# Kernel optimization log

Measured on AMD Instinct MI355X. Metric: run time of the kernel, lower is better.

## Reference

```python
import jax, jax.numpy as jnp
import numpy as np
import math

B, S, E = 4, 1024, 1024
H = 16
HD = E // H            # 64
HD2 = HD // 2          # 32
DEPTH = 12 - 1
LAMBDA_INIT = 0.8 - 0.6 * math.exp(-0.3 * DEPTH)
EPS = 1e-5


def setup_inputs() -> dict:
    key = jax.random.key(0)
    ks = jax.random.split(key, 16)
    std = 1.0 / math.sqrt(E)
    inp = {
        "hidden_states": jax.random.normal(ks[0], (B, S, E), jnp.float32),
        "q_w": jax.random.normal(ks[1], (E, E), jnp.float32) * std,
        "q_b": jnp.zeros((E,), jnp.float32),
        "k_w": jax.random.normal(ks[2], (E, E), jnp.float32) * std,
        "k_b": jnp.zeros((E,), jnp.float32),
        "v_w": jax.random.normal(ks[3], (E, E), jnp.float32) * std,
        "v_b": jnp.zeros((E,), jnp.float32),
        "o_w": jax.random.normal(ks[4], (E, E), jnp.float32) * std,
        "o_b": jnp.zeros((E,), jnp.float32),
        "lambda_q1": jax.random.normal(ks[5], (HD2,), jnp.float32) * 0.1,
        "lambda_k1": jax.random.normal(ks[6], (HD2,), jnp.float32) * 0.1,
        "lambda_q2": jax.random.normal(ks[7], (HD2,), jnp.float32) * 0.1,
        "lambda_k2": jax.random.normal(ks[8], (HD2,), jnp.float32) * 0.1,
        "subln_w": jnp.ones((HD,), jnp.float32),
    }
    return inp


def reference(hidden_states, q_w, q_b, k_w, k_b, v_w, v_b, o_w, o_b,
              lambda_q1, lambda_k1, lambda_q2, lambda_k2, subln_w):
    b, s, _ = hidden_states.shape
    # projections (torch Linear: x @ W.T + b)
    q = hidden_states @ q_w.T + q_b
    k = hidden_states @ k_w.T + k_b
    v = hidden_states @ v_w.T + v_b
    # split q/k into 2*H heads of dim HD2; v into H heads of dim HD
    q = q.reshape(b, s, 2 * H, HD2).transpose(0, 2, 1, 3)   # [B,2H,S,HD2]
    k = k.reshape(b, s, 2 * H, HD2).transpose(0, 2, 1, 3)   # [B,2H,S,HD2]
    v = v.reshape(b, s, H, HD).transpose(0, 2, 1, 3)        # [B,H,S,HD]
    # scores scaled by sqrt(head_dim) (full head_dim, per source)
    scores = jnp.einsum('bhqd,bhkd->bhqk', q, k) / math.sqrt(HD)
    scores = jnp.nan_to_num(scores)
    attn_w = jax.nn.softmax(scores.astype(jnp.float32), axis=-1).astype(scores.dtype)
    lam1 = jnp.exp(jnp.sum(lambda_q1 * lambda_k1))
    lam2 = jnp.exp(jnp.sum(lambda_q2 * lambda_k2))
    lam = lam1 - lam2 + LAMBDA_INIT
    attn_w = attn_w.reshape(b, H, 2, s, s)
    diff_w = attn_w[:, :, 0] - lam * attn_w[:, :, 1]        # [B,H,S,S]
    attn = jnp.einsum('bhqk,bhkd->bhqd', diff_w, v)          # [B,H,S,HD]
    # RMSNorm over head dim, elementwise affine
    attn = attn * jax.lax.rsqrt(jnp.mean(attn * attn, axis=-1, keepdims=True) + EPS) * subln_w
    attn = attn * (1.0 - LAMBDA_INIT)
    attn = attn.transpose(0, 2, 1, 3).reshape(b, s, H * HD)
    out = attn @ o_w.T + o_b
    return out, diff_w
```

## Files before the change

### kernel.cpp

```cpp
#include <hip/hip_runtime.h>

typedef __attribute__((ext_vector_type(8))) short short8;
typedef __attribute__((ext_vector_type(4))) float floatx4;

#define MFMA16(a, b, c) __builtin_amdgcn_mfma_f32_16x16x32_bf16((a), (b), (c), 0, 0, 0)

#define LAMBDA_INIT_F 0.777870099559256f
#define ONE_MINUS_LAMBDA_F 0.222129900440744f

static __device__ __forceinline__ unsigned short f2bf(float f) {
  union { float f; unsigned int u; } v; v.f = f;
  unsigned int r = v.u + 0x7FFFu + ((v.u >> 16) & 1u);
  return (unsigned short)(r >> 16);
}

__global__ __launch_bounds__(256) void cvt_f32_bf16(const float* __restrict__ in,
                                                    unsigned short* __restrict__ out,
                                                    int n) {
  int i = blockIdx.x * 256 + threadIdx.x;
  if (i < n) out[i] = f2bf(in[i]);
}

template <int MODE>
__global__ __launch_bounds__(256) void gemm_bt(const unsigned short* __restrict__ A,
                                               const unsigned short* __restrict__ Bt,
                                               const float* __restrict__ bias,
                                               void* __restrict__ out,
                                               int M, int N, int K) {
  __shared__ unsigned short As[64][40];
  __shared__ unsigned short Bs[64][40];
  const int tid = threadIdx.x;
  const int m0 = blockIdx.y * 64;
  const int n0 = blockIdx.x * 64;
  const int w = tid >> 6, lane = tid & 63;
  const int wm = (w >> 1) * 32, wn = (w & 1) * 32;
  const int lrow = lane & 15, quad = lane >> 4;

  floatx4 acc[2][2];
  for (int i = 0; i < 2; i++)
    for (int j = 0; j < 2; j++)
      acc[i][j] = (floatx4){0.f, 0.f, 0.f, 0.f};

  const int ldr = tid >> 2;
  const int ldc = (tid & 3) * 8;

  for (int k0 = 0; k0 < K; k0 += 32) {
    short8 av = *(const short8*)(A + (size_t)(m0 + ldr) * K + k0 + ldc);
    short8 bv = *(const short8*)(Bt + (size_t)(n0 + ldr) * K + k0 + ldc);
    *(short8*)(&As[ldr][ldc]) = av;
    *(short8*)(&Bs[ldr][ldc]) = bv;
    __syncthreads();
    short8 a0 = *(const short8*)(&As[wm + lrow][quad * 8]);
    short8 a1 = *(const short8*)(&As[wm + 16 + lrow][quad * 8]);
    short8 b0 = *(const short8*)(&Bs[wn + lrow][quad * 8]);
    short8 b1 = *(const short8*)(&Bs[wn + 16 + lrow][quad * 8]);
    acc[0][0] = MFMA16(a0, b0, acc[0][0]);
    acc[0][1] = MFMA16(a0, b1, acc[0][1]);
    acc[1][0] = MFMA16(a1, b0, acc[1][0]);
    acc[1][1] = MFMA16(a1, b1, acc[1][1]);
    __syncthreads();
  }

  for (int mi = 0; mi < 2; mi++)
    for (int ni = 0; ni < 2; ni++)
      for (int r = 0; r < 4; r++) {
        int row = m0 + wm + mi * 16 + quad * 4 + r;
        int col = n0 + wn + ni * 16 + lrow;
        float v = acc[mi][ni][r] + bias[col];
        if (MODE == 1) {
          int b = row >> 10, s = row & 1023, h2 = col >> 5, d = col & 31;
          ((unsigned short*)out)[((((size_t)(b * 32 + h2)) << 10) + s) * 32 + d] = f2bf(v);
        } else if (MODE == 2) {
          int b = row >> 10, s = row & 1023, h = col >> 6, d = col & 63;
          ((unsigned short*)out)[((((size_t)(b * 16 + h)) * 64 + d) << 10) + s] = f2bf(v);
        } else {
          ((float*)out)[(size_t)row * N + col] = v;
        }
      }
}

__global__ __launch_bounds__(256) void attn_stats(const unsigned short* __restrict__ qh,
                                                  const unsigned short* __restrict__ kh,
                                                  float* __restrict__ stat_m,
                                                  float* __restrict__ stat_l) {
  const int W = blockIdx.x * 4 + (threadIdx.x >> 6);
  const int lane = threadIdx.x & 63;
  const int chunk = W & 63;
  const int bh = W >> 6;
  const int b = bh >> 4, h = bh & 15;
  const int lrow = lane & 15, quad = lane >> 4;
  const int r0 = chunk * 16;

  const unsigned short* q1 = qh + ((((size_t)(b * 32 + 2 * h)) << 10) + r0) * 32;
  const unsigned short* q2 = qh + ((((size_t)(b * 32 + 2 * h + 1)) << 10) + r0) * 32;
  const unsigned short* k1 = kh + (((size_t)(b * 32 + 2 * h)) << 10) * 32;
  const unsigned short* k2 = kh + (((size_t)(b * 32 + 2 * h + 1)) << 10) * 32;

  short8 a1 = *(const short8*)(q1 + lrow * 32 + quad * 8);
  short8 a2 = *(const short8*)(q2 + lrow * 32 + quad * 8);

  float m1[4], l1[4], m2[4], l2[4];
  for (int r = 0; r < 4; r++) { m1[r] = -1e30f; l1[r] = 0.f; m2[r] = -1e30f; l2[r] = 0.f; }

  for (int c = 0; c < 64; c++) {
    short8 bk1 = *(const short8*)(k1 + (c * 16 + lrow) * 32 + quad * 8);
    short8 bk2 = *(const short8*)(k2 + (c * 16 + lrow) * 32 + quad * 8);
    floatx4 z = (floatx4){0.f, 0.f, 0.f, 0.f};
    floatx4 s1 = MFMA16(a1, bk1, z);
    floatx4 s2 = MFMA16(a2, bk2, z);
    for (int r = 0; r < 4; r++) {
      float v1 = s1[r] * 0.125f;
      float nm1 = fmaxf(m1[r], v1);
      l1[r] = l1[r] * __expf(m1[r] - nm1) + __expf(v1 - nm1);
      m1[r] = nm1;
      float v2 = s2[r] * 0.125f;
      float nm2 = fmaxf(m2[r], v2);
      l2[r] = l2[r] * __expf(m2[r] - nm2) + __expf(v2 - nm2);
      m2[r] = nm2;
    }
  }
  for (int off = 1; off < 16; off <<= 1) {
    for (int r = 0; r < 4; r++) {
      float om = __shfl_xor(m1[r], off);
      float ol = __shfl_xor(l1[r], off);
      float nm = fmaxf(m1[r], om);
      l1[r] = l1[r] * __expf(m1[r] - nm) + ol * __expf(om - nm);
      m1[r] = nm;
      om = __shfl_xor(m2[r], off);
      ol = __shfl_xor(l2[r], off);
      nm = fmaxf(m2[r], om);
      l2[r] = l2[r] * __expf(m2[r] - nm) + ol * __expf(om - nm);
      m2[r] = nm;
    }
  }
  if (lrow == 0) {
    for (int r = 0; r < 4; r++) {
      int row = r0 + quad * 4 + r;
      size_t i1 = (((size_t)(b * 32 + 2 * h)) << 10) + row;
      size_t i2 = (((size_t)(b * 32 + 2 * h + 1)) << 10) + row;
      stat_m[i1] = m1[r]; stat_l[i1] = l1[r];
      stat_m[i2] = m2[r]; stat_l[i2] = l2[r];
    }
  }
}

__global__ __launch_bounds__(256) void attn_pass2(const unsigned short* __restrict__ qh,
                                                  const unsigned short* __restrict__ kh,
                                                  const unsigned short* __restrict__ vt,
                                                  const float* __restrict__ stat_m,
                                                  const float* __restrict__ stat_l,
                                                  const float* __restrict__ lq1,
                                                  const float* __restrict__ lk1,
                                                  const float* __restrict__ lq2,
                                                  const float* __restrict__ lk2,
                                                  const float* __restrict__ subln,
                                                  float* __restrict__ diffw,
                                                  unsigned short* __restrict__ attn_out) {
  __shared__ unsigned short ds[4][16][40];
  const int wid = threadIdx.x >> 6;
  const int W = blockIdx.x * 4 + wid;
  const int lane = threadIdx.x & 63;
  const int chunk = W & 63;
  const int bh = W >> 6;
  const int b = bh >> 4, h = bh & 15;
  const int lrow = lane & 15, quad = lane >> 4;
  const int r0 = chunk * 16;

  float sl1 = 0.f, sl2 = 0.f;
  for (int i = 0; i < 32; i++) { sl1 += lq1[i] * lk1[i]; sl2 += lq2[i] * lk2[i]; }
  const float lam = __expf(sl1) - __expf(sl2) + LAMBDA_INIT_F;

  const unsigned short* q1 = qh + ((((size_t)(b * 32 + 2 * h)) << 10) + r0) * 32;
  const unsigned short* q2 = qh + ((((size_t)(b * 32 + 2 * h + 1)) << 10) + r0) * 32;
  const unsigned short* k1 = kh + (((size_t)(b * 32 + 2 * h)) << 10) * 32;
  const unsigned short* k2 = kh + (((size_t)(b * 32 + 2 * h + 1)) << 10) * 32;
  const unsigned short* vth = vt + (((size_t)(b * 16 + h)) << 16);

  short8 a1 = *(const short8*)(q1 + lrow * 32 + quad * 8);
  short8 a2 = *(const short8*)(q2 + lrow * 32 + quad * 8);

  float em1[4], il1[4], em2[4], il2[4];
  for (int r = 0; r < 4; r++) {
    int row = r0 + quad * 4 + r;
    size_t i1 = (((size_t)(b * 32 + 2 * h)) << 10) + row;
    size_t i2 = (((size_t)(b * 32 + 2 * h + 1)) << 10) + row;
    em1[r] = stat_m[i1]; il1[r] = 1.f / stat_l[i1];
    em2[r] = stat_m[i2]; il2[r] = 1.f / stat_l[i2];
  }

  floatx4 accO[4];
  for (int nt = 0; nt < 4; nt++) accO[nt] = (floatx4){0.f, 0.f, 0.f, 0.f};

  float* dwbase = diffw + (((size_t)bh) << 20) + (size_t)r0 * 1024;

  for (int c2 = 0; c2 < 32; c2++) {
    for (int cc = 0; cc < 2; cc++) {
      int c = c2 * 2 + cc;
      short8 bk1 = *(const short8*)(k1 + (c * 16 + lrow) * 32 + quad * 8);
      short8 bk2 = *(const short8*)(k2 + (c * 16 + lrow) * 32 + quad * 8);
      floatx4 z = (floatx4){0.f, 0.f, 0.f, 0.f};
      floatx4 s1 = MFMA16(a1, bk1, z);
      floatx4 s2 = MFMA16(a2, bk2, z);
      for (int r = 0; r < 4; r++) {
        float p1 = __expf(s1[r] * 0.125f - em1[r]) * il1[r];
        float p2 = __expf(s2[r] * 0.125f - em2[r]) * il2[r];
        float d = p1 - lam * p2;
        dwbase[(size_t)(quad * 4 + r) * 1024 + c * 16 + lrow] = d;
        ds[wid][quad * 4 + r][cc * 16 + lrow] = f2bf(d);
      }
    }
    short8 ad = *(const short8*)(&ds[wid][lrow][quad * 8]);
    for (int nt = 0; nt < 4; nt++) {
      short8 bv = *(const short8*)(vth + (((size_t)(nt * 16 + lrow)) << 10) + c2 * 32 + quad * 8);
      accO[nt] = MFMA16(ad, bv, accO[nt]);
    }
  }

  float rs[4];
  for (int r = 0; r < 4; r++) {
    float s = 0.f;
    for (int nt = 0; nt < 4; nt++) s += accO[nt][r] * accO[nt][r];
    for (int off = 1; off < 16; off <<= 1) s += __shfl_xor(s, off);
    rs[r] = rsqrtf(s * (1.f / 64.f) + 1e-5f);
  }
  for (int r = 0; r < 4; r++) {
    int row = r0 + quad * 4 + r;
    for (int nt = 0; nt < 4; nt++) {
      int d = nt * 16 + lrow;
      float v = accO[nt][r] * rs[r] * subln[d] * ONE_MINUS_LAMBDA_F;
      attn_out[((((size_t)b) << 10) + row) * 1024 + h * 64 + d] = f2bf(v);
    }
  }
}

extern "C" void kernel_launch(void* const* d_in, const int* in_sizes, int n_in,
                              void* d_out, int out_size, void* d_ws, size_t ws_size,
                              hipStream_t stream) {
  (void)in_sizes; (void)n_in; (void)out_size; (void)ws_size;
  const float* hs = (const float*)d_in[0];
  const float* q_w = (const float*)d_in[1];
  const float* q_b = (const float*)d_in[2];
  const float* k_w = (const float*)d_in[3];
  const float* k_b = (const float*)d_in[4];
  const float* v_w = (const float*)d_in[5];
  const float* v_b = (const float*)d_in[6];
  const float* o_w = (const float*)d_in[7];
  const float* o_b = (const float*)d_in[8];
  const float* lq1 = (const float*)d_in[9];
  const float* lk1 = (const float*)d_in[10];
  const float* lq2 = (const float*)d_in[11];
  const float* lk2 = (const float*)d_in[12];
  const float* subln = (const float*)d_in[13];

  char* ws = (char*)d_ws;
  unsigned short* hs_bf = (unsigned short*)(ws + 0);
  unsigned short* qw_bf = (unsigned short*)(ws + 8388608);
  unsigned short* kw_bf = (unsigned short*)(ws + 10485760);
  unsigned short* vw_bf = (unsigned short*)(ws + 12582912);
  unsigned short* ow_bf = (unsigned short*)(ws + 14680064);
  unsigned short* q_h = (unsigned short*)(ws + 16777216);
  unsigned short* k_h = (unsigned short*)(ws + 25165824);
  unsigned short* v_t = (unsigned short*)(ws + 33554432);
  unsigned short* attnb = (unsigned short*)(ws + 41943040);
  float* stat_m = (float*)(ws + 50331648);
  float* stat_l = (float*)(ws + 50855936);

  cvt_f32_bf16<<<16384, 256, 0, stream>>>(hs, hs_bf, 4194304);
  cvt_f32_bf16<<<4096, 256, 0, stream>>>(q_w, qw_bf, 1048576);
  cvt_f32_bf16<<<4096, 256, 0, stream>>>(k_w, kw_bf, 1048576);
  cvt_f32_bf16<<<4096, 256, 0, stream>>>(v_w, vw_bf, 1048576);
  cvt_f32_bf16<<<4096, 256, 0, stream>>>(o_w, ow_bf, 1048576);

  gemm_bt<1><<<dim3(16, 64), 256, 0, stream>>>(hs_bf, qw_bf, q_b, (void*)q_h, 4096, 1024, 1024);
  gemm_bt<1><<<dim3(16, 64), 256, 0, stream>>>(hs_bf, kw_bf, k_b, (void*)k_h, 4096, 1024, 1024);
  gemm_bt<2><<<dim3(16, 64), 256, 0, stream>>>(hs_bf, vw_bf, v_b, (void*)v_t, 4096, 1024, 1024);

  attn_stats<<<1024, 256, 0, stream>>>(q_h, k_h, stat_m, stat_l);

  float* outf = (float*)d_out;
  attn_pass2<<<1024, 256, 0, stream>>>(q_h, k_h, v_t, stat_m, stat_l,
                                       lq1, lk1, lq2, lk2, subln,
                                       outf + 4194304, attnb);

  gemm_bt<3><<<dim3(16, 64), 256, 0, stream>>>(attnb, ow_bf, o_b, (void*)outf, 4096, 1024, 1024);
}
```

Baseline: 573.3 us.

## Rewrite pipeline: fused QKV GEMM, single-pass attention, larger GEMM tiles

Replaces the three separate QKV GEMMs with one 128x128-tile GEMM that loads global memory straight into LDS, and stores V in natural layout followed by a separate transpose kernel. The two-pass attention (stats kernel plus recompute) becomes a single kernel. Each block splits the key range across four waves, keeps the scores in registers, and reduces max, sum and the output across waves through shared memory. The conversion kernels are vectorised to float4 and the attention output buffer reuses the hidden-state workspace. This removes the duplicated QK^T and exp work and raises GEMM data reuse, at the cost of higher register pressure and an extra transpose pass.

```diff
diff --git a/kernel.cpp b/kernel.cpp
--- a/kernel.cpp
+++ b/kernel.cpp
@@ -7,6 +7,11 @@
 
 #define LAMBDA_INIT_F 0.777870099559256f
 #define ONE_MINUS_LAMBDA_F 0.222129900440744f
+
+#define GLL(g, l)                                                              \
+  __builtin_amdgcn_global_load_lds(                                            \
+      (const __attribute__((address_space(1))) void*)(g),                      \
+      (__attribute__((address_space(3))) void*)(l), 16, 0, 0)
 
 static __device__ __forceinline__ unsigned short f2bf(float f) {
   union { float f; unsigned int u; } v; v.f = f;
@@ -16,220 +21,337 @@
 
 __global__ __launch_bounds__(256) void cvt_f32_bf16(const float* __restrict__ in,
                                                     unsigned short* __restrict__ out,
-                                                    int n) {
+                                                    int n4) {
   int i = blockIdx.x * 256 + threadIdx.x;
-  if (i < n) out[i] = f2bf(in[i]);
-}
-
-template <int MODE>
-__global__ __launch_bounds__(256) void gemm_bt(const unsigned short* __restrict__ A,
-                                               const unsigned short* __restrict__ Bt,
-                                               const float* __restrict__ bias,
-                                               void* __restrict__ out,
-                                               int M, int N, int K) {
-  __shared__ unsigned short As[64][40];
-  __shared__ unsigned short Bs[64][40];
+  if (i < n4) {
+    float4 v = ((const float4*)in)[i];
+    unsigned short o0 = f2bf(v.x), o1 = f2bf(v.y), o2 = f2bf(v.z), o3 = f2bf(v.w);
+    ushort2 a = {o0, o1}, b = {o2, o3};
+    ((ushort2*)out)[i * 2] = a;
+    ((ushort2*)out)[i * 2 + 1] = b;
+  }
+}
+
+__device__ __forceinline__ void gemm128_core(const unsigned short* __restrict__ A,
+                                             const unsigned short* __restrict__ Bt,
+                                             unsigned short* As, unsigned short* Bs,
+                                             int m0, int n0, floatx4 (&acc)[4][4]) {
   const int tid = threadIdx.x;
-  const int m0 = blockIdx.y * 64;
-  const int n0 = blockIdx.x * 64;
   const int w = tid >> 6, lane = tid & 63;
-  const int wm = (w >> 1) * 32, wn = (w & 1) * 32;
   const int lrow = lane & 15, quad = lane >> 4;
-
-  floatx4 acc[2][2];
-  for (int i = 0; i < 2; i++)
-    for (int j = 0; j < 2; j++)
+  const int wm = (w >> 1) * 64, wn = (w & 1) * 64;
+
+#pragma unroll
+  for (int i = 0; i < 4; i++)
+#pragma unroll
+    for (int j = 0; j < 4; j++)
       acc[i][j] = (floatx4){0.f, 0.f, 0.f, 0.f};
 
-  const int ldr = tid >> 2;
-  const int ldc = (tid & 3) * 8;
-
-  for (int k0 = 0; k0 < K; k0 += 32) {
-    short8 av = *(const short8*)(A + (size_t)(m0 + ldr) * K + k0 + ldc);
-    short8 bv = *(const short8*)(Bt + (size_t)(n0 + ldr) * K + k0 + ldc);
-    *(short8*)(&As[ldr][ldc]) = av;
-    *(short8*)(&Bs[ldr][ldc]) = bv;
+  const int ar = tid >> 2;
+  const int ac = (tid & 3) * 8;
+  const unsigned short* ga = A + (size_t)(m0 + ar) * 1024 + ac;
+  const unsigned short* gb = Bt + (size_t)(n0 + ar) * 1024 + ac;
+  unsigned short* la = As + w * 512;
+  unsigned short* lb = Bs + w * 512;
+
+  for (int k0 = 0; k0 < 1024; k0 += 32) {
+    GLL(ga + k0, la);
+    GLL(ga + k0 + 64 * 1024, la + 2048);
+    GLL(gb + k0, lb);
+    GLL(gb + k0 + 64 * 1024, lb + 2048);
     __syncthreads();
-    short8 a0 = *(const short8*)(&As[wm + lrow][quad * 8]);
-    short8 a1 = *(const short8*)(&As[wm + 16 + lrow][quad * 8]);
-    short8 b0 = *(const short8*)(&Bs[wn + lrow][quad * 8]);
-    short8 b1 = *(const short8*)(&Bs[wn + 16 + lrow][quad * 8]);
-    acc[0][0] = MFMA16(a0, b0, acc[0][0]);
-    acc[0][1] = MFMA16(a0, b1, acc[0][1]);
-    acc[1][0] = MFMA16(a1, b0, acc[1][0]);
-    acc[1][1] = MFMA16(a1, b1, acc[1][1]);
+    short8 af[4], bfr[4];
+#pragma unroll
+    for (int i = 0; i < 4; i++)
+      af[i] = *(const short8*)(As + (wm + i * 16 + lrow) * 32 + quad * 8);
+#pragma unroll
+    for (int j = 0; j < 4; j++)
+      bfr[j] = *(const short8*)(Bs + (wn + j * 16 + lrow) * 32 + quad * 8);
+#pragma unroll
+    for (int i = 0; i < 4; i++)
+#pragma unroll
+      for (int j = 0; j < 4; j++)
+        acc[i][j] = MFMA16(af[i], bfr[j], acc[i][j]);
     __syncthreads();
   }
-
-  for (int mi = 0; mi < 2; mi++)
-    for (int ni = 0; ni < 2; ni++)
+}
+
+__global__ __launch_bounds__(256, 2) void gemm_qkv(const unsigned short* __restrict__ A,
+                                                   const unsigned short* __restrict__ qw,
+                                                   const unsigned short* __restrict__ kw,
+                                                   const unsigned short* __restrict__ vw,
+                                                   const float* __restrict__ qb,
+                                                   const float* __restrict__ kb,
+                                                   const float* __restrict__ vb,
+                                                   unsigned short* __restrict__ qh,
+                                                   unsigned short* __restrict__ kh,
+                                                   unsigned short* __restrict__ vnat) {
+  __shared__ unsigned short As[128 * 32];
+  __shared__ unsigned short Bs[128 * 32];
+  const int m0 = blockIdx.y * 128;
+  const int nglob = blockIdx.x * 128;
+  const int wsel = nglob >> 10;
+  const int nloc = nglob & 1023;
+  const unsigned short* Bt = (wsel == 0) ? qw : ((wsel == 1) ? kw : vw);
+  const float* bias = (wsel == 0) ? qb : ((wsel == 1) ? kb : vb);
+
+  floatx4 acc[4][4];
+  gemm128_core(A, Bt, As, Bs, m0, nloc, acc);
+
+  const int tid = threadIdx.x;
+  const int w = tid >> 6, lane = tid & 63;
+  const int lrow = lane & 15, quad = lane >> 4;
+  const int wm = (w >> 1) * 64, wn = (w & 1) * 64;
+
+#pragma unroll
+  for (int i = 0; i < 4; i++)
+#pragma unroll
+    for (int j = 0; j < 4; j++) {
+      int col = nloc + wn + j * 16 + lrow;
+      float bcol = bias[col];
+#pragma unroll
       for (int r = 0; r < 4; r++) {
-        int row = m0 + wm + mi * 16 + quad * 4 + r;
-        int col = n0 + wn + ni * 16 + lrow;
-        float v = acc[mi][ni][r] + bias[col];
-        if (MODE == 1) {
+        int row = m0 + wm + i * 16 + quad * 4 + r;
+        float v = acc[i][j][r] + bcol;
+        if (wsel < 2) {
           int b = row >> 10, s = row & 1023, h2 = col >> 5, d = col & 31;
-          ((unsigned short*)out)[((((size_t)(b * 32 + h2)) << 10) + s) * 32 + d] = f2bf(v);
-        } else if (MODE == 2) {
-          int b = row >> 10, s = row & 1023, h = col >> 6, d = col & 63;
-          ((unsigned short*)out)[((((size_t)(b * 16 + h)) * 64 + d) << 10) + s] = f2bf(v);
+          unsigned short* o = (wsel == 0) ? qh : kh;
+          o[((((size_t)(b * 32 + h2)) << 10) + s) * 32 + d] = f2bf(v);
         } else {
-          ((float*)out)[(size_t)row * N + col] = v;
+          vnat[(size_t)row * 1024 + col] = f2bf(v);
         }
       }
-}
-
-__global__ __launch_bounds__(256) void attn_stats(const unsigned short* __restrict__ qh,
-                                                  const unsigned short* __restrict__ kh,
-                                                  float* __restrict__ stat_m,
-                                                  float* __restrict__ stat_l) {
-  const int W = blockIdx.x * 4 + (threadIdx.x >> 6);
-  const int lane = threadIdx.x & 63;
-  const int chunk = W & 63;
-  const int bh = W >> 6;
-  const int b = bh >> 4, h = bh & 15;
+    }
+}
+
+__global__ __launch_bounds__(256, 2) void gemm_o(const unsigned short* __restrict__ A,
+                                                 const unsigned short* __restrict__ ow,
+                                                 const float* __restrict__ ob,
+                                                 float* __restrict__ out) {
+  __shared__ unsigned short As[128 * 32];
+  __shared__ unsigned short Bs[128 * 32];
+  const int m0 = blockIdx.y * 128;
+  const int n0 = blockIdx.x * 128;
+
+  floatx4 acc[4][4];
+  gemm128_core(A, ow, As, Bs, m0, n0, acc);
+
+  const int tid = threadIdx.x;
+  const int w = tid >> 6, lane = tid & 63;
   const int lrow = lane & 15, quad = lane >> 4;
-  const int r0 = chunk * 16;
-
-  const unsigned short* q1 = qh + ((((size_t)(b * 32 + 2 * h)) << 10) + r0) * 32;
-  const unsigned short* q2 = qh + ((((size_t)(b * 32 + 2 * h + 1)) << 10) + r0) * 32;
-  const unsigned short* k1 = kh + (((size_t)(b * 32 + 2 * h)) << 10) * 32;
-  const unsigned short* k2 = kh + (((size_t)(b * 32 + 2 * h + 1)) << 10) * 32;
-
-  short8 a1 = *(const short8*)(q1 + lrow * 32 + quad * 8);
-  short8 a2 = *(const short8*)(q2 + lrow * 32 + quad * 8);
-
-  float m1[4], l1[4], m2[4], l2[4];
-  for (int r = 0; r < 4; r++) { m1[r] = -1e30f; l1[r] = 0.f; m2[r] = -1e30f; l2[r] = 0.f; }
-
-  for (int c = 0; c < 64; c++) {
-    short8 bk1 = *(const short8*)(k1 + (c * 16 + lrow) * 32 + quad * 8);
-    short8 bk2 = *(const short8*)(k2 + (c * 16 + lrow) * 32 + quad * 8);
-    floatx4 z = (floatx4){0.f, 0.f, 0.f, 0.f};
-    floatx4 s1 = MFMA16(a1, bk1, z);
-    floatx4 s2 = MFMA16(a2, bk2, z);
-    for (int r = 0; r < 4; r++) {
-      float v1 = s1[r] * 0.125f;
-      float nm1 = fmaxf(m1[r], v1);
-      l1[r] = l1[r] * __expf(m1[r] - nm1) + __expf(v1 - nm1);
-      m1[r] = nm1;
-      float v2 = s2[r] * 0.125f;
-      float nm2 = fmaxf(m2[r], v2);
-      l2[r] = l2[r] * __expf(m2[r] - nm2) + __expf(v2 - nm2);
-      m2[r] = nm2;
-    }
-  }
-  for (int off = 1; off < 16; off <<= 1) {
-    for (int r = 0; r < 4; r++) {
-      float om = __shfl_xor(m1[r], off);
-      float ol = __shfl_xor(l1[r], off);
-      float nm = fmaxf(m1[r], om);
-      l1[r] = l1[r] * __expf(m1[r] - nm) + ol * __expf(om - nm);
-      m1[r] = nm;
-      om = __shfl_xor(m2[r], off);
-      ol = __shfl_xor(l2[r], off);
-      nm = fmaxf(m2[r], om);
-      l2[r] = l2[r] * __expf(m2[r] - nm) + ol * __expf(om - nm);
-      m2[r] = nm;
-    }
-  }
-  if (lrow == 0) {
-    for (int r = 0; r < 4; r++) {
-      int row = r0 + quad * 4 + r;
-      size_t i1 = (((size_t)(b * 32 + 2 * h)) << 10) + row;
-      size_t i2 = (((size_t)(b * 32 + 2 * h + 1)) << 10) + row;
-      stat_m[i1] = m1[r]; stat_l[i1] = l1[r];
-      stat_m[i2] = m2[r]; stat_l[i2] = l2[r];
-    }
-  }
-}
-
-__global__ __launch_bounds__(256) void attn_pass2(const unsigned short* __restrict__ qh,
+  const int wm = (w >> 1) * 64, wn = (w & 1) * 64;
+
+#pragma unroll
+  for (int i = 0; i < 4; i++)
+#pragma unroll
+    for (int j = 0; j < 4; j++) {
+      int col = n0 + wn + j * 16 + lrow;
+      float bcol = ob[col];
+#pragma unroll
+      for (int r = 0; r < 4; r++) {
+        int row = m0 + wm + i * 16 + quad * 4 + r;
+        out[(size_t)row * 1024 + col] = acc[i][j][r] + bcol;
+      }
+    }
+}
+
+__global__ __launch_bounds__(256) void transpose_v(const unsigned short* __restrict__ vn,
+                                                   unsigned short* __restrict__ vt) {
+  __shared__ unsigned int tile[64][65];
+  const int t = threadIdx.x;
+  const int bh = blockIdx.y, b = bh >> 4, h = bh & 15;
+  const int s0 = blockIdx.x * 64;
+#pragma unroll
+  for (int i = 0; i < 2; i++) {
+    int r = i * 32 + (t >> 3);
+    int c8 = (t & 7) * 8;
+    short8 v = *(const short8*)(vn + ((size_t)(b * 1024 + s0 + r)) * 1024 + h * 64 + c8);
+#pragma unroll
+    for (int j = 0; j < 8; j++) tile[r][c8 + j] = (unsigned short)v[j];
+  }
+  __syncthreads();
+  const int w = t >> 6, lane = t & 63;
+#pragma unroll
+  for (int dd = 0; dd < 16; dd++) {
+    int d = w * 16 + dd;
+    unsigned short u = (unsigned short)tile[lane][d];
+    vt[(((size_t)(b * 16 + h)) * 64 + d) * 1024 + s0 + lane] = u;
+  }
+}
+
+__global__ __launch_bounds__(256) void attn_fused(const unsigned short* __restrict__ qh,
                                                   const unsigned short* __restrict__ kh,
                                                   const unsigned short* __restrict__ vt,
-                                                  const float* __restrict__ stat_m,
-                                                  const float* __restrict__ stat_l,
                                                   const float* __restrict__ lq1,
                                                   const float* __restrict__ lk1,
                                                   const float* __restrict__ lq2,
                                                   const float* __restrict__ lk2,
                                                   const float* __restrict__ subln,
                                                   float* __restrict__ diffw,
-                                                  unsigned short* __restrict__ attn_out) {
-  __shared__ unsigned short ds[4][16][40];
-  const int wid = threadIdx.x >> 6;
-  const int W = blockIdx.x * 4 + wid;
-  const int lane = threadIdx.x & 63;
-  const int chunk = W & 63;
-  const int bh = W >> 6;
+                                                  unsigned short* __restrict__ attnb) {
+  __shared__ float redm[4][2][16];
+  __shared__ float redl[4][2][16];
+  __shared__ unsigned short dsA[4][16][40];
+  __shared__ float ored[4][16][64];
+
+  const int tid = threadIdx.x;
+  const int w = tid >> 6, lane = tid & 63;
+  const int lrow = lane & 15, quad = lane >> 4;
+  const int blk = blockIdx.x;
+  const int chunk = blk & 63, bh = blk >> 6;
   const int b = bh >> 4, h = bh & 15;
-  const int lrow = lane & 15, quad = lane >> 4;
   const int r0 = chunk * 16;
+  const int cbase = w * 256;
 
   float sl1 = 0.f, sl2 = 0.f;
   for (int i = 0; i < 32; i++) { sl1 += lq1[i] * lk1[i]; sl2 += lq2[i] * lk2[i]; }
   const float lam = __expf(sl1) - __expf(sl2) + LAMBDA_INIT_F;
 
   const unsigned short* q1 = qh + ((((size_t)(b * 32 + 2 * h)) << 10) + r0) * 32;
-  const unsigned short* q2 = qh + ((((size_t)(b * 32 + 2 * h + 1)) << 10) + r0) * 32;
+  const unsigned short* q2 = q1 + (32u << 10);
   const unsigned short* k1 = kh + (((size_t)(b * 32 + 2 * h)) << 10) * 32;
-  const unsigned short* k2 = kh + (((size_t)(b * 32 + 2 * h + 1)) << 10) * 32;
+  const unsigned short* k2 = k1 + (32u << 10);
   const unsigned short* vth = vt + (((size_t)(b * 16 + h)) << 16);
 
   short8 a1 = *(const short8*)(q1 + lrow * 32 + quad * 8);
   short8 a2 = *(const short8*)(q2 + lrow * 32 + quad * 8);
 
-  float em1[4], il1[4], em2[4], il2[4];
+  floatx4 s1a[16], s2a[16];
+  float m1[4], m2[4];
+#pragma unroll
+  for (int r = 0; r < 4; r++) { m1[r] = -1e30f; m2[r] = -1e30f; }
+
+  const floatx4 zero = (floatx4){0.f, 0.f, 0.f, 0.f};
+
+#pragma unroll
+  for (int ct = 0; ct < 16; ct++) {
+    short8 bk = *(const short8*)(k1 + (size_t)(cbase + ct * 16 + lrow) * 32 + quad * 8);
+    floatx4 s = MFMA16(a1, bk, zero);
+#pragma unroll
+    for (int r = 0; r < 4; r++) {
+      float v = s[r] * 0.125f;
+      s1a[ct][r] = v;
+      m1[r] = fmaxf(m1[r], v);
+    }
+  }
+#pragma unroll
+  for (int ct = 0; ct < 16; ct++) {
+    short8 bk = *(const short8*)(k2 + (size_t)(cbase + ct * 16 + lrow) * 32 + quad * 8);
+    floatx4 s = MFMA16(a2, bk, zero);
+#pragma unroll
+    for (int r = 0; r < 4; r++) {
+      float v = s[r] * 0.125f;
+      s2a[ct][r] = v;
+      m2[r] = fmaxf(m2[r], v);
+    }
+  }
+
+#pragma unroll
+  for (int off = 1; off < 16; off <<= 1) {
+#pragma unroll
+    for (int r = 0; r < 4; r++) {
+      m1[r] = fmaxf(m1[r], __shfl_xor(m1[r], off));
+      m2[r] = fmaxf(m2[r], __shfl_xor(m2[r], off));
+    }
+  }
+  if (lrow == 0) {
+#pragma unroll
+    for (int r = 0; r < 4; r++) {
+      redm[w][0][quad * 4 + r] = m1[r];
+      redm[w][1][quad * 4 + r] = m2[r];
+    }
+  }
+  __syncthreads();
+  float mf1[4], mf2[4];
+#pragma unroll
   for (int r = 0; r < 4; r++) {
-    int row = r0 + quad * 4 + r;
-    size_t i1 = (((size_t)(b * 32 + 2 * h)) << 10) + row;
-    size_t i2 = (((size_t)(b * 32 + 2 * h + 1)) << 10) + row;
-    em1[r] = stat_m[i1]; il1[r] = 1.f / stat_l[i1];
-    em2[r] = stat_m[i2]; il2[r] = 1.f / stat_l[i2];
+    int rr = quad * 4 + r;
+    mf1[r] = fmaxf(fmaxf(redm[0][0][rr], redm[1][0][rr]), fmaxf(redm[2][0][rr], redm[3][0][rr]));
+    mf2[r] = fmaxf(fmaxf(redm[0][1][rr], redm[1][1][rr]), fmaxf(redm[2][1][rr], redm[3][1][rr]));
+  }
+
+  float l1[4] = {0.f, 0.f, 0.f, 0.f}, l2[4] = {0.f, 0.f, 0.f, 0.f};
+#pragma unroll
+  for (int ct = 0; ct < 16; ct++) {
+#pragma unroll
+    for (int r = 0; r < 4; r++) {
+      float e1 = __expf(s1a[ct][r] - mf1[r]);
+      s1a[ct][r] = e1;
+      l1[r] += e1;
+      float e2 = __expf(s2a[ct][r] - mf2[r]);
+      s2a[ct][r] = e2;
+      l2[r] += e2;
+    }
+  }
+#pragma unroll
+  for (int off = 1; off < 16; off <<= 1) {
+#pragma unroll
+    for (int r = 0; r < 4; r++) {
+      l1[r] += __shfl_xor(l1[r], off);
+      l2[r] += __shfl_xor(l2[r], off);
+    }
+  }
+  if (lrow == 0) {
+#pragma unroll
+    for (int r = 0; r < 4; r++) {
+      redl[w][0][quad * 4 + r] = l1[r];
+      redl[w][1][quad * 4 + r] = l2[r];
+    }
+  }
+  __syncthreads();
+  float il1[4], il2[4];
+#pragma unroll
+  for (int r = 0; r < 4; r++) {
+    int rr = quad * 4 + r;
+    il1[r] = 1.f / (redl[0][0][rr] + redl[1][0][rr] + redl[2][0][rr] + redl[3][0][rr]);
+    il2[r] = 1.f / (redl[0][1][rr] + redl[1][1][rr] + redl[2][1][rr] + redl[3][1][rr]);
   }
 
   floatx4 accO[4];
-  for (int nt = 0; nt < 4; nt++) accO[nt] = (floatx4){0.f, 0.f, 0.f, 0.f};
-
-  float* dwbase = diffw + (((size_t)bh) << 20) + (size_t)r0 * 1024;
-
-  for (int c2 = 0; c2 < 32; c2++) {
+#pragma unroll
+  for (int nt = 0; nt < 4; nt++) accO[nt] = zero;
+
+  float* dwbase = diffw + (((size_t)bh) << 20) + (size_t)r0 * 1024 + cbase;
+
+#pragma unroll
+  for (int c2 = 0; c2 < 8; c2++) {
+#pragma unroll
     for (int cc = 0; cc < 2; cc++) {
-      int c = c2 * 2 + cc;
-      short8 bk1 = *(const short8*)(k1 + (c * 16 + lrow) * 32 + quad * 8);
-      short8 bk2 = *(const short8*)(k2 + (c * 16 + lrow) * 32 + quad * 8);
-      floatx4 z = (floatx4){0.f, 0.f, 0.f, 0.f};
-      floatx4 s1 = MFMA16(a1, bk1, z);
-      floatx4 s2 = MFMA16(a2, bk2, z);
+      int ct = c2 * 2 + cc;
+#pragma unroll
       for (int r = 0; r < 4; r++) {
-        float p1 = __expf(s1[r] * 0.125f - em1[r]) * il1[r];
-        float p2 = __expf(s2[r] * 0.125f - em2[r]) * il2[r];
+        float p1 = s1a[ct][r] * il1[r];
+        float p2 = s2a[ct][r] * il2[r];
         float d = p1 - lam * p2;
-        dwbase[(size_t)(quad * 4 + r) * 1024 + c * 16 + lrow] = d;
-        ds[wid][quad * 4 + r][cc * 16 + lrow] = f2bf(d);
+        dwbase[(size_t)(quad * 4 + r) * 1024 + ct * 16 + lrow] = d;
+        dsA[w][quad * 4 + r][cc * 16 + lrow] = f2bf(d);
       }
     }
-    short8 ad = *(const short8*)(&ds[wid][lrow][quad * 8]);
+    short8 ad = *(const short8*)(&dsA[w][lrow][quad * 8]);
+#pragma unroll
     for (int nt = 0; nt < 4; nt++) {
-      short8 bv = *(const short8*)(vth + (((size_t)(nt * 16 + lrow)) << 10) + c2 * 32 + quad * 8);
+      short8 bv = *(const short8*)(vth + (size_t)(nt * 16 + lrow) * 1024 + cbase + c2 * 32 + quad * 8);
       accO[nt] = MFMA16(ad, bv, accO[nt]);
     }
   }
 
-  float rs[4];
-  for (int r = 0; r < 4; r++) {
-    float s = 0.f;
-    for (int nt = 0; nt < 4; nt++) s += accO[nt][r] * accO[nt][r];
-    for (int off = 1; off < 16; off <<= 1) s += __shfl_xor(s, off);
-    rs[r] = rsqrtf(s * (1.f / 64.f) + 1e-5f);
-  }
-  for (int r = 0; r < 4; r++) {
-    int row = r0 + quad * 4 + r;
-    for (int nt = 0; nt < 4; nt++) {
-      int d = nt * 16 + lrow;
-      float v = accO[nt][r] * rs[r] * subln[d] * ONE_MINUS_LAMBDA_F;
-      attn_out[((((size_t)b) << 10) + row) * 1024 + h * 64 + d] = f2bf(v);
-    }
+#pragma unroll
+  for (int nt = 0; nt < 4; nt++)
+#pragma unroll
+    for (int r = 0; r < 4; r++)
+      ored[w][quad * 4 + r][nt * 16 + lrow] = accO[nt][r];
+  __syncthreads();
+
+#pragma unroll
+  for (int rr = 0; rr < 4; rr++) {
+    int row = w * 4 + rr;
+    float o = ored[0][row][lane] + ored[1][row][lane] + ored[2][row][lane] + ored[3][row][lane];
+    float ss = o * o;
+#pragma unroll
+    for (int off = 1; off < 64; off <<= 1) ss += __shfl_xor(ss, off);
+    float rs = rsqrtf(ss * (1.f / 64.f) + 1e-5f);
+    float v = o * rs * subln[lane] * ONE_MINUS_LAMBDA_F;
+    attnb[((((size_t)b) << 10) + r0 + row) * 1024 + h * 64 + lane] = f2bf(v);
   }
 }
 
@@ -254,33 +376,30 @@
 
   char* ws = (char*)d_ws;
   unsigned short* hs_bf = (unsigned short*)(ws + 0);
+  unsigned short* attnb = (unsigned short*)(ws + 0);
   unsigned short* qw_bf = (unsigned short*)(ws + 8388608);
   unsigned short* kw_bf = (unsigned short*)(ws + 10485760);
   unsigned short* vw_bf = (unsigned short*)(ws + 12582912);
   unsigned short* ow_bf = (unsigned short*)(ws + 14680064);
   unsigned short* q_h = (unsigned short*)(ws + 16777216);
   unsigned short* k_h = (unsigned short*)(ws + 25165824);
-  unsigned short* v_t = (unsigned short*)(ws + 33554432);
-  unsigned short* attnb = (unsigned short*)(ws + 41943040);
-  float* stat_m = (float*)(ws + 50331648);
-  float* stat_l = (float*)(ws + 50855936);
-
-  cvt_f32_bf16<<<16384, 256, 0, stream>>>(hs, hs_bf, 4194304);
-  cvt_f32_bf16<<<4096, 256, 0, stream>>>(q_w, qw_bf, 1048576);
-  cvt_f32_bf16<<<4096, 256, 0, stream>>>(k_w, kw_bf, 1048576);
-  cvt_f32_bf16<<<4096, 256, 0, stream>>>(v_w, vw_bf, 1048576);
-  cvt_f32_bf16<<<4096, 256, 0, stream>>>(o_w, ow_bf, 1048576);
-
-  gemm_bt<1><<<dim3(16, 64), 256, 0, stream>>>(hs_bf, qw_bf, q_b, (void*)q_h, 4096, 1024, 1024);
-  gemm_bt<1><<<dim3(16, 64), 256, 0, stream>>>(hs_bf, kw_bf, k_b, (void*)k_h, 4096, 1024, 1024);
-  gemm_bt<2><<<dim3(16, 64), 256, 0, stream>>>(hs_bf, vw_bf, v_b, (void*)v_t, 4096, 1024, 1024);
-
-  attn_stats<<<1024, 256, 0, stream>>>(q_h, k_h, stat_m, stat_l);
+  unsigned short* v_nat = (unsigned short*)(ws + 33554432);
+  unsigned short* v_t = (unsigned short*)(ws + 41943040);
+
+  cvt_f32_bf16<<<4096, 256, 0, stream>>>(hs, hs_bf, 1048576);
+  cvt_f32_bf16<<<1024, 256, 0, stream>>>(q_w, qw_bf, 262144);
+  cvt_f32_bf16<<<1024, 256, 0, stream>>>(k_w, kw_bf, 262144);
+  cvt_f32_bf16<<<1024, 256, 0, stream>>>(v_w, vw_bf, 262144);
+  cvt_f32_bf16<<<1024, 256, 0, stream>>>(o_w, ow_bf, 262144);
+
+  gemm_qkv<<<dim3(24, 32), 256, 0, stream>>>(hs_bf, qw_bf, kw_bf, vw_bf,
+                                             q_b, k_b, v_b, q_h, k_h, v_nat);
+
+  transpose_v<<<dim3(16, 64), 256, 0, stream>>>(v_nat, v_t);
 
   float* outf = (float*)d_out;
-  attn_pass2<<<1024, 256, 0, stream>>>(q_h, k_h, v_t, stat_m, stat_l,
-                                       lq1, lk1, lq2, lk2, subln,
+  attn_fused<<<4096, 256, 0, stream>>>(q_h, k_h, v_t, lq1, lk1, lq2, lk2, subln,
                                        outf + 4194304, attnb);
 
-  gemm_bt<3><<<dim3(16, 64), 256, 0, stream>>>(attnb, ow_bf, o_b, (void*)outf, 4096, 1024, 1024);
-}
+  gemm_o<<<dim3(8, 32), 256, 0, stream>>>(attnb, ow_bf, o_b, outf);
+}
```

Measured after the change: 538.0 us. -6.2%, faster.
